# Optimization experiments

Hardware: AMD Instinct MI355X
Metric: run time of the kernel (lower is better)

## Reference

```python
import jax, jax.numpy as jnp
import numpy as np

NEG = jnp.float32(-1e30)

def setup_inputs() -> dict:
    key = jax.random.key(0)
    k1, k2, k3, k4, k5, k6 = jax.random.split(key, 6)
    B, L, P, D = 16, 512, 32, 256
    inputs = jax.random.normal(k1, (B, L, D), dtype=jnp.float32)
    left_paths = jax.random.randint(k2, (B, L, P), 0, L)
    right_paths = jax.random.randint(k3, (B, L, P), 0, L)
    # path lengths >= 1 (a path always contains at least one node)
    left_lens = jax.random.randint(k4, (B, L), 1, P + 1)
    right_lens = jax.random.randint(k5, (B, L), 1, P + 1)
    sent_lens = jax.random.randint(k6, (B,), 1, L + 1)
    return {"inputs": inputs, "left_paths": left_paths, "right_paths": right_paths,
            "left_lens": left_lens, "right_lens": right_lens, "sent_lens": sent_lens}

def _path_max(inputs, paths, lens):
    # inputs: [B,L,D]; paths: [B,L,P]; lens: [B,L] -> masked max over path dim: [B,L,D]
    B = inputs.shape[0]
    P = paths.shape[-1]
    b_idx = jnp.arange(B)[:, None, None]
    gathered = inputs[b_idx, paths]                      # [B,L,P,D]
    mask = jnp.arange(P)[None, None, :] < lens[..., None]  # [B,L,P]
    return jnp.max(jnp.where(mask[..., None], gathered, NEG), axis=2)

def reference(inputs, left_paths, right_paths, left_lens, right_lens, sent_lens):
    L = inputs.shape[1]
    left_max = _path_max(inputs, left_paths, left_lens)    # [B,L,D]
    right_max = _path_max(inputs, right_paths, right_lens)  # [B,L,D]
    out = jnp.concatenate([left_max, right_max], axis=-1)   # [B,L,2D]
    token_mask = jnp.arange(L)[None, :] < sent_lens[:, None]  # zero-pad past sentence length
    return jnp.where(token_mask[..., None], out, 0.0)
```

## Files before the change

kernel.cpp:

```cpp
#include <hip/hip_runtime.h>


constexpr int BB = 16;
constexpr int LL = 512;
constexpr int PP = 32;
constexpr int D4 = 64;

__device__ __forceinline__ float4 f4max(float4 a, float4 b) {
    return make_float4(fmaxf(a.x, b.x), fmaxf(a.y, b.y),
                       fmaxf(a.z, b.z), fmaxf(a.w, b.w));
}

__global__ __launch_bounds__(128) void encoder_sdp_kernel(
    const float4* __restrict__ inputs,
    const int*    __restrict__ left_paths,
    const int*    __restrict__ right_paths,
    const int*    __restrict__ left_lens,
    const int*    __restrict__ right_lens,
    const int*    __restrict__ sent_lens,
    float4*       __restrict__ out)
{
    const int blk  = blockIdx.x;
    const int b    = blk & (BB - 1);
    const int l    = blk >> 4;
    const int t    = threadIdx.x;
    const int side = t >> 6;
    const int lane = t & 63;
    const int bl   = b * LL + l;

    float4* outp = out + (size_t)bl * (2 * D4) + side * D4 + lane;

    if (l >= sent_lens[b]) {
        *outp = make_float4(0.f, 0.f, 0.f, 0.f);
        return;
    }

    const int* paths = side ? right_paths : left_paths;
    const int* lens  = side ? right_lens  : left_lens;
    const int  len   = lens[bl];
    const int  myidx = paths[(size_t)bl * PP + (lane & (PP - 1))];

    const float4* base = inputs + (size_t)b * LL * D4 + lane;

    const float NEGV = -1e30f;
    float4 a0 = make_float4(NEGV, NEGV, NEGV, NEGV);
    float4 a1 = a0, a2 = a0, a3 = a0;

    int p = 0;
    for (; p + 4 <= len; p += 4) {
        const int i0 = __shfl(myidx, p + 0, 64);
        const int i1 = __shfl(myidx, p + 1, 64);
        const int i2 = __shfl(myidx, p + 2, 64);
        const int i3 = __shfl(myidx, p + 3, 64);
        const float4 v0 = base[(size_t)i0 * D4];
        const float4 v1 = base[(size_t)i1 * D4];
        const float4 v2 = base[(size_t)i2 * D4];
        const float4 v3 = base[(size_t)i3 * D4];
        a0 = f4max(a0, v0);
        a1 = f4max(a1, v1);
        a2 = f4max(a2, v2);
        a3 = f4max(a3, v3);
    }
    for (; p < len; ++p) {
        const int i0 = __shfl(myidx, p, 64);
        a0 = f4max(a0, base[(size_t)i0 * D4]);
    }

    a0 = f4max(f4max(a0, a1), f4max(a2, a3));
    *outp = a0;
}

extern "C" void kernel_launch(void* const* d_in, const int* in_sizes, int n_in,
                              void* d_out, int out_size, void* d_ws, size_t ws_size,
                              hipStream_t stream) {
    const float4* inputs      = (const float4*)d_in[0];
    const int*    left_paths  = (const int*)d_in[1];
    const int*    right_paths = (const int*)d_in[2];
    const int*    left_lens   = (const int*)d_in[3];
    const int*    right_lens  = (const int*)d_in[4];
    const int*    sent_lens   = (const int*)d_in[5];
    float4*       out         = (float4*)d_out;

    encoder_sdp_kernel<<<BB * LL, 128, 0, stream>>>(
        inputs, left_paths, right_paths, left_lens, right_lens, sent_lens, out);
}
```

Before: 83.72 us.

## Split sides into separate one-wave blocks, use scalar index loads and nontemporal stores

```diff
diff --git a/kernel.cpp b/kernel.cpp
--- a/kernel.cpp
+++ b/kernel.cpp
@@ -6,81 +6,85 @@
 constexpr int PP = 32;
 constexpr int D4 = 64;
 
-__device__ __forceinline__ float4 f4max(float4 a, float4 b) {
-    return make_float4(fmaxf(a.x, b.x), fmaxf(a.y, b.y),
-                       fmaxf(a.z, b.z), fmaxf(a.w, b.w));
+typedef float v4f __attribute__((ext_vector_type(4)));
+
+__device__ __forceinline__ v4f v4max(v4f a, v4f b) {
+    v4f r;
+    r.x = fmaxf(a.x, b.x);
+    r.y = fmaxf(a.y, b.y);
+    r.z = fmaxf(a.z, b.z);
+    r.w = fmaxf(a.w, b.w);
+    return r;
 }
 
-__global__ __launch_bounds__(128) void encoder_sdp_kernel(
-    const float4* __restrict__ inputs,
-    const int*    __restrict__ left_paths,
-    const int*    __restrict__ right_paths,
-    const int*    __restrict__ left_lens,
-    const int*    __restrict__ right_lens,
-    const int*    __restrict__ sent_lens,
-    float4*       __restrict__ out)
+__global__ __launch_bounds__(64) void encoder_sdp_kernel(
+    const v4f* __restrict__ inputs,
+    const int* __restrict__ left_paths,
+    const int* __restrict__ right_paths,
+    const int* __restrict__ left_lens,
+    const int* __restrict__ right_lens,
+    const int* __restrict__ sent_lens,
+    v4f*       __restrict__ out)
 {
     const int blk  = blockIdx.x;
+    const int side = blockIdx.y;
     const int b    = blk & (BB - 1);
     const int l    = blk >> 4;
-    const int t    = threadIdx.x;
-    const int side = t >> 6;
-    const int lane = t & 63;
+    const int lane = threadIdx.x;
     const int bl   = b * LL + l;
 
-    float4* outp = out + (size_t)bl * (2 * D4) + side * D4 + lane;
+    v4f* outp = out + (size_t)bl * (2 * D4) + side * D4 + lane;
 
     if (l >= sent_lens[b]) {
-        *outp = make_float4(0.f, 0.f, 0.f, 0.f);
+        v4f z = {0.f, 0.f, 0.f, 0.f};
+        __builtin_nontemporal_store(z, outp);
         return;
     }
 
     const int* paths = side ? right_paths : left_paths;
     const int* lens  = side ? right_lens  : left_lens;
     const int  len   = lens[bl];
-    const int  myidx = paths[(size_t)bl * PP + (lane & (PP - 1))];
+    const int* pbase = paths + (size_t)bl * PP;
 
-    const float4* base = inputs + (size_t)b * LL * D4 + lane;
+    const v4f* base = inputs + (size_t)b * LL * D4 + lane;
 
     const float NEGV = -1e30f;
-    float4 a0 = make_float4(NEGV, NEGV, NEGV, NEGV);
-    float4 a1 = a0, a2 = a0, a3 = a0;
+    v4f a0 = {NEGV, NEGV, NEGV, NEGV};
+    v4f a1 = a0, a2 = a0, a3 = a0;
 
-    int p = 0;
-    for (; p + 4 <= len; p += 4) {
-        const int i0 = __shfl(myidx, p + 0, 64);
-        const int i1 = __shfl(myidx, p + 1, 64);
-        const int i2 = __shfl(myidx, p + 2, 64);
-        const int i3 = __shfl(myidx, p + 3, 64);
-        const float4 v0 = base[(size_t)i0 * D4];
-        const float4 v1 = base[(size_t)i1 * D4];
-        const float4 v2 = base[(size_t)i2 * D4];
-        const float4 v3 = base[(size_t)i3 * D4];
-        a0 = f4max(a0, v0);
-        a1 = f4max(a1, v1);
-        a2 = f4max(a2, v2);
-        a3 = f4max(a3, v3);
-    }
-    for (; p < len; ++p) {
-        const int i0 = __shfl(myidx, p, 64);
-        a0 = f4max(a0, base[(size_t)i0 * D4]);
+    const int lm1 = len - 1;
+    const int nch = (len + 3) >> 2;
+    for (int c = 0; c < nch; ++c) {
+        const int p  = c << 2;
+        const int i0 = pbase[p];
+        const int i1 = pbase[min(p + 1, lm1)];
+        const int i2 = pbase[min(p + 2, lm1)];
+        const int i3 = pbase[min(p + 3, lm1)];
+        const v4f v0 = base[(size_t)i0 * D4];
+        const v4f v1 = base[(size_t)i1 * D4];
+        const v4f v2 = base[(size_t)i2 * D4];
+        const v4f v3 = base[(size_t)i3 * D4];
+        a0 = v4max(a0, v0);
+        a1 = v4max(a1, v1);
+        a2 = v4max(a2, v2);
+        a3 = v4max(a3, v3);
     }
 
-    a0 = f4max(f4max(a0, a1), f4max(a2, a3));
-    *outp = a0;
+    a0 = v4max(v4max(a0, a1), v4max(a2, a3));
+    __builtin_nontemporal_store(a0, outp);
 }
 
 extern "C" void kernel_launch(void* const* d_in, const int* in_sizes, int n_in,
                               void* d_out, int out_size, void* d_ws, size_t ws_size,
                               hipStream_t stream) {
-    const float4* inputs      = (const float4*)d_in[0];
-    const int*    left_paths  = (const int*)d_in[1];
-    const int*    right_paths = (const int*)d_in[2];
-    const int*    left_lens   = (const int*)d_in[3];
-    const int*    right_lens  = (const int*)d_in[4];
-    const int*    sent_lens   = (const int*)d_in[5];
-    float4*       out         = (float4*)d_out;
+    const v4f* inputs      = (const v4f*)d_in[0];
+    const int* left_paths  = (const int*)d_in[1];
+    const int* right_paths = (const int*)d_in[2];
+    const int* left_lens   = (const int*)d_in[3];
+    const int* right_lens  = (const int*)d_in[4];
+    const int* sent_lens   = (const int*)d_in[5];
+    v4f*       out         = (v4f*)d_out;
 
-    encoder_sdp_kernel<<<BB * LL, 128, 0, stream>>>(
+    encoder_sdp_kernel<<<dim3(BB * LL, 2), 64, 0, stream>>>(
         inputs, left_paths, right_paths, left_lens, right_lens, sent_lens, out);
 }
```

Result: faster. 81.93 us (-2.1%).
